# Kernel tuning notes

Measured on AMD Instinct MI355X. Metric: run time of the kernel, lower is better.

The kernel has to match this reference:

```python
import jax, jax.numpy as jnp
import numpy as np

KS = 3
N = KS ** 3  # 27 kernel taps
EPS = 1e-5

def conv3d(x, w, stride=1, padding=0):
    return jax.lax.conv_general_dilated(
        x, w, (stride,) * 3, [(padding, padding)] * 3,
        dimension_numbers=('NCDHW', 'OIDHW', 'NCDHW'))

def batchnorm(x, gamma, beta):
    mu = jnp.mean(x, axis=(0, 2, 3, 4), keepdims=True)
    var = jnp.var(x, axis=(0, 2, 3, 4), keepdims=True)
    return (x - mu) * jax.lax.rsqrt(var + EPS) * gamma[None, :, None, None, None] + beta[None, :, None, None, None]

def deform_conv3d(x, w_p, b_p, w_m, b_m, w_dc):
    b, c, D, H, W = x.shape
    offset = conv3d(x, w_p, padding=1) + b_p[None, :, None, None, None]      # (b,3N,D,H,W)
    m = jax.nn.sigmoid(conv3d(x, w_m, padding=1) + b_m[None, :, None, None, None])  # (b,N,D,H,W)
    x_pad = jnp.pad(x, ((0, 0), (0, 0), (1, 1), (1, 1), (1, 1)))
    Dp, Hp, Wp = D + 2, H + 2, W + 2
    r = jnp.arange(-(KS - 1) // 2, KS // 2 + 1, dtype=x.dtype)
    pn_d, pn_h, pn_w = [a.reshape(-1) for a in jnp.meshgrid(r, r, r, indexing='ij')]
    off = offset.transpose(0, 2, 3, 4, 1)                                    # (b,D,H,W,3N)
    p0_d = jnp.arange(1, D + 1, dtype=x.dtype)[:, None, None, None]
    p0_h = jnp.arange(1, H + 1, dtype=x.dtype)[None, :, None, None]
    p0_w = jnp.arange(1, W + 1, dtype=x.dtype)[None, None, :, None]
    pd = p0_d + pn_d + off[..., :N]
    ph = p0_h + pn_h + off[..., N:2 * N]
    pw = p0_w + pn_w + off[..., 2 * N:]
    d0 = jnp.clip(jnp.floor(pd), 0.0, Dp - 1.0); d1 = jnp.clip(d0 + 1.0, 0.0, Dp - 1.0)
    h0 = jnp.clip(jnp.floor(ph), 0.0, Hp - 1.0); h1 = jnp.clip(h0 + 1.0, 0.0, Hp - 1.0)
    w0 = jnp.clip(jnp.floor(pw), 0.0, Wp - 1.0); w1 = jnp.clip(w0 + 1.0, 0.0, Wp - 1.0)
    pd = jnp.clip(pd, 0.0, Dp - 1.0); ph = jnp.clip(ph, 0.0, Hp - 1.0); pw = jnp.clip(pw, 0.0, Wp - 1.0)
    xf = x_pad.reshape(b, c, -1)
    def gather(qd, qh, qw):
        idx = (qd * (Hp * Wp) + qh * Wp + qw).astype(jnp.int32).reshape(b, 1, -1)
        v = jnp.take_along_axis(xf, jnp.broadcast_to(idx, (b, c, idx.shape[-1])), axis=2)
        return v.reshape(b, c, D, H, W, N)
    x_off = jnp.zeros((b, c, D, H, W, N), x.dtype)
    for qd, wd in ((d0, 1.0 + d0 - pd), (d1, 1.0 - d1 + pd)):
        for qh, wh in ((h0, 1.0 + h0 - ph), (h1, 1.0 - h1 + ph)):
            for qw, ww in ((w0, 1.0 + w0 - pw), (w1, 1.0 - w1 + pw)):
                x_off = x_off + (wd * wh * ww)[:, None] * gather(qd, qh, qw)
    x_off = x_off * m.transpose(0, 2, 3, 4, 1)[:, None]                      # modulation
    # interleave kernel taps: (b,c,D,kd,H,kh,W,kw) -> (b,c,D*KS,H*KS,W*KS)
    x_off = x_off.reshape(b, c, D, H, W, KS, KS, KS)
    x_off = x_off.transpose(0, 1, 2, 5, 3, 6, 4, 7).reshape(b, c, D * KS, H * KS, W * KS)
    out = conv3d(x_off, w_dc, stride=KS)
    p = jnp.concatenate([pd, ph, pw], axis=-1)                               # (b,D,H,W,3N)
    return out, p

def setup_inputs() -> dict:
    key = jax.random.key(0)
    ks = jax.random.split(key, 10)
    B, D = 4, 48
    return {
        'x': jax.random.normal(ks[0], (B, 1, D, D, D), jnp.float32),
        'w_p': jax.random.normal(ks[1], (3 * N, 1, KS, KS, KS), jnp.float32) * 0.05,
        'b_p': jnp.zeros((3 * N,), jnp.float32),
        'w_m': jax.random.normal(ks[2], (N, 1, KS, KS, KS), jnp.float32) * 0.1,
        'b_m': jnp.zeros((N,), jnp.float32),
        'w_dc': jax.random.normal(ks[3], (1, 1, KS, KS, KS), jnp.float32) * 0.2,
        'g_d': jnp.ones((1,), jnp.float32), 'be_d': jnp.zeros((1,), jnp.float32),
        'w_c1': jax.random.normal(ks[4], (32, 1, KS, KS, KS), jnp.float32) * 0.3,
        'g1': jnp.ones((32,), jnp.float32), 'be1': jnp.zeros((32,), jnp.float32),
        'w_c2': jax.random.normal(ks[5], (64, 32, KS, KS, KS), jnp.float32) * 0.06,
        'g2': jnp.ones((64,), jnp.float32), 'be2': jnp.zeros((64,), jnp.float32),
        'w_fc': jax.random.normal(ks[6], (10, 64), jnp.float32) * 0.1,
        'b_fc': jnp.zeros((10,), jnp.float32),
    }

def reference(x, w_p, b_p, w_m, b_m, w_dc, g_d, be_d, w_c1, g1, be1, w_c2, g2, be2, w_fc, b_fc):
    inp = x
    for _ in range(2):
        y, p = deform_conv3d(inp, w_p, b_p, w_m, b_m, w_dc)
        xxx = y
        inp = jax.nn.relu(batchnorm(y, g_d, be_d))
    h = jax.nn.relu(batchnorm(conv3d(inp, w_c1, padding=1), g1, be1))
    h = jax.nn.relu(batchnorm(conv3d(h, w_c2, padding=1), g2, be2))
    h = jax.lax.reduce_window(h, -jnp.inf, jax.lax.max, (1, 1, 3, 3, 3), (1, 1, 3, 3, 3), 'VALID')
    h = h.mean(axis=(2, 3, 4))                       # adaptive avg pool to 1
    logits = h @ w_fc.T + b_fc
    return logits, xxx, p
```

## Files before the change

kernel.cpp:

```cpp
#include <hip/hip_runtime.h>
#include <math.h>

#define BSZ 4
#define DD 48
#define SS (48*48*48)
#define NV (BSZ*SS)
#define PS 125000
#define EPSBN 1e-5f

typedef __attribute__((ext_vector_type(8))) short bf16x8;
typedef __attribute__((ext_vector_type(4))) short s16x4;
typedef __attribute__((ext_vector_type(4))) float f32x4;

__device__ __forceinline__ short f2b(float f){
  unsigned u = __float_as_uint(f);
  u = (u + 0x7FFFu + ((u>>16)&1u)) >> 16;
  return (short)u;
}
__device__ __forceinline__ float b2f(short s){
  return __uint_as_float(((unsigned)(unsigned short)s)<<16);
}

__global__ __launch_bounds__(256) void pad_kernel(
    const float* __restrict__ src, float* __restrict__ dst)
{
  int idx = blockIdx.x*256 + threadIdx.x;
  if (idx >= BSZ*PS) return;
  int b = idx / PS; int r = idx - b*PS;
  int z = r/2500; int r2 = r - z*2500; int yy = r2/50; int xx = r2 - yy*50;
  float v = 0.f;
  if (z>=1 && z<=48 && yy>=1 && yy<=48 && xx>=1 && xx<=48)
    v = src[(size_t)b*SS + (size_t)((z-1)*48 + (yy-1))*48 + (xx-1)];
  dst[idx] = v;
}

__global__ void woff2_kernel(const float* __restrict__ w_p, const float* __restrict__ b_p,
                             const float* __restrict__ w_m, const float* __restrict__ b_m,
                             short* __restrict__ wo2)
{
  int o = blockIdx.x*256 + threadIdx.x;
  if (o >= 112*32) return;
  int k = o & 31; int c = o >> 5;
  int f = c >> 4, qq = (c >> 2) & 3, r = c & 3;
  int n = 4*f + qq;
  float v = 0.f;
  if (n < 27){
    if (k < 27)       v = (r < 3) ? w_p[(r*27+n)*27 + k] : w_m[n*27 + k];
    else if (k == 27) v = (r < 3) ? b_p[r*27+n]          : b_m[n];
  }
  wo2[o] = f2b(v);
}

template<bool WRITE_P>
__global__ __launch_bounds__(256) void deform3_kernel(
    const float* __restrict__ xpad,
    const short* __restrict__ wo2,
    const float* __restrict__ w_dc,
    float* __restrict__ y, float* __restrict__ p_out)
{
  __shared__ short xt[6*6*18];
  __shared__ __align__(16) float pbuf[WRITE_P ? 64*81 : 4];

  int bid = blockIdx.x;
  int bw = bid % 3; int bh = (bid/3)%12; int bd = (bid/36)%12; int b = bid/432;
  int d0 = bd*4, h0 = bh*4, w0 = bw*16;
  int tid = threadIdx.x;
  const float* xp = xpad + (size_t)b*PS;

  for (int e = tid; e < 648; e += 256){
    int z = e/108; int rem = e - z*108; int yy = rem/18; int xx = rem - yy*18;
    xt[e] = f2b(xp[(d0+z)*2500 + (h0+yy)*50 + (w0+xx)]);
  }
  __syncthreads();

  int lane = tid & 63, wid = tid >> 6;
  int q = lane >> 4, n16 = lane & 15;

  bf16x8 aF[7];
  #pragma unroll
  for (int f=0; f<7; ++f)
    aF[f] = *(const bf16x8*)(wo2 + (f*16 + n16)*32 + q*8);

  int toffs[8];
  #pragma unroll
  for (int j=0;j<8;++j){
    int t = q*8 + j; int tc = t > 26 ? 0 : t;
    int kd = tc/9, rr = tc - kd*9, kh = rr/3, kw = rr - kh*3;
    toffs[j] = kd*108 + kh*18 + kw;
  }

  float wdcv[7], fkd[7], fkh[7], fkw[7];
  #pragma unroll
  for (int f=0; f<7; ++f){
    int n = 4*f + q;
    if (n < 27){
      int kd = n/9, rr = n - kd*9, kh = rr/3, kw = rr - kh*3;
      wdcv[f] = w_dc[n];
      fkd[f] = (float)kd; fkh[f] = (float)kh; fkw[f] = (float)kw;
    } else { wdcv[f]=0.f; fkd[f]=0.f; fkh[f]=0.f; fkw[f]=0.f; }
  }

  const short one_bf = (short)0x3F80;
  const f32x4 zero4 = {0.f,0.f,0.f,0.f};
  float based = (float)(d0 + wid);
  float basew = (float)(w0 + n16);

  #pragma unroll 1
  for (int dy=0; dy<4; ++dy){
    int vbase = wid*108 + dy*18 + n16;
    bf16x8 bF;
    #pragma unroll
    for (int j=0;j<8;++j){
      short xv = xt[vbase + toffs[j]];
      bF[j] = (j<3 || q<3) ? xv : one_bf;
    }
    f32x4 acc[7];
    #pragma unroll
    for (int f=0; f<7; ++f)
      acc[f] = __builtin_amdgcn_mfma_f32_16x16x32_bf16(aF[f], bF, zero4, 0,0,0);

    float baseh = (float)(h0 + dy);
    float accv = 0.f;
    #pragma unroll
    for (int f=0; f<7; ++f){
      int n = 4*f + q;
      if (n < 27){
        float od = acc[f][0], oh = acc[f][1], ow = acc[f][2], mr = acc[f][3];
        float mm = __builtin_amdgcn_rcpf(1.f + __expf(-mr));
        float pdv = based + fkd[f] + od;
        float phv = baseh + fkh[f] + oh;
        float pwv = basew + fkw[f] + ow;
        float fd0 = fminf(fmaxf(floorf(pdv),0.f),49.f), fd1 = fminf(fd0+1.f,49.f);
        float pdc = fminf(fmaxf(pdv,0.f),49.f);
        float wd0 = 1.f + fd0 - pdc, wd1 = 1.f - fd1 + pdc;
        float fh0 = fminf(fmaxf(floorf(phv),0.f),49.f), fh1 = fminf(fh0+1.f,49.f);
        float phc = fminf(fmaxf(phv,0.f),49.f);
        float wh0 = 1.f + fh0 - phc, wh1 = 1.f - fh1 + phc;
        float fw0 = fminf(fmaxf(floorf(pwv),0.f),49.f), fw1 = fminf(fw0+1.f,49.f);
        float pwc = fminf(fmaxf(pwv,0.f),49.f);
        float wwa = 1.f + fw0 - pwc, wwb = 1.f - fw1 + pwc;
        int iz0 = (int)fd0*2500, iz1 = (int)fd1*2500;
        int iy0 = (int)fh0*50,   iy1 = (int)fh1*50;
        int ix0 = (int)fw0,      ix1 = (int)fw1;
        float v000=xp[iz0+iy0+ix0], v001=xp[iz0+iy0+ix1];
        float v010=xp[iz0+iy1+ix0], v011=xp[iz0+iy1+ix1];
        float v100=xp[iz1+iy0+ix0], v101=xp[iz1+iy0+ix1];
        float v110=xp[iz1+iy1+ix0], v111=xp[iz1+iy1+ix1];
        float sv = wd0*(wh0*(wwa*v000+wwb*v001)+wh1*(wwa*v010+wwb*v011))
                 + wd1*(wh0*(wwa*v100+wwb*v101)+wh1*(wwa*v110+wwb*v111));
        accv += sv*mm*wdcv[f];
        if constexpr (WRITE_P){
          int vb = (wid*16 + n16)*81;
          pbuf[vb + n]      = pdc;
          pbuf[vb + 27 + n] = phc;
          pbuf[vb + 54 + n] = pwc;
        }
      }
    }
    accv += __shfl_xor(accv, 16);
    accv += __shfl_xor(accv, 32);
    if (q == 0)
      y[(size_t)b*SS + (size_t)((d0+wid)*48 + (h0+dy))*48 + (w0+n16)] = accv;

    if constexpr (WRITE_P){
      __syncthreads();
      size_t rbase = ((((size_t)b*48 + (d0+wid))*48 + (h0+dy))*48 + w0)*81;
      const float* src = pbuf + wid*1296;
      float* dst = p_out + rbase;
      #pragma unroll
      for (int k=0;k<6;++k){
        int i4 = (lane + (k<<6))<<2;
        if (i4 < 1296){
          f32x4 v = *(const f32x4*)(src + i4);
          *(f32x4*)(dst + i4) = v;
        }
      }
      __syncthreads();
    }
  }
}

__global__ __launch_bounds__(256) void bn_stats_kernel(
    const float* __restrict__ x, int nch, float* __restrict__ sums)
{
  int c = blockIdx.y;
  float s1=0.f, s2=0.f;
  for (int i=blockIdx.x*blockDim.x+threadIdx.x; i<NV; i+=gridDim.x*blockDim.x){
    int b=i/SS; int s=i-b*SS;
    float v = x[((size_t)b*nch+c)*SS + s];
    s1+=v; s2+=v*v;
  }
  __shared__ float r1[256], r2[256];
  r1[threadIdx.x]=s1; r2[threadIdx.x]=s2; __syncthreads();
  for (int o=128;o>0;o>>=1){
    if (threadIdx.x<o){ r1[threadIdx.x]+=r1[threadIdx.x+o]; r2[threadIdx.x]+=r2[threadIdx.x+o]; }
    __syncthreads();
  }
  if (threadIdx.x==0){ atomicAdd(&sums[2*c],r1[0]); atomicAdd(&sums[2*c+1],r2[0]); }
}

__global__ __launch_bounds__(256) void bn_relu_kernel(
    const float* __restrict__ x, float* __restrict__ out,
    const float* __restrict__ sums, const float* __restrict__ gamma,
    const float* __restrict__ beta, int nch)
{
  size_t idx = (size_t)blockIdx.x*blockDim.x + threadIdx.x;
  size_t total = (size_t)BSZ*nch*SS;
  if (idx>=total) return;
  int c = (int)((idx/SS)%nch);
  float mu  = sums[2*c]  *(1.f/(float)NV);
  float var = sums[2*c+1]*(1.f/(float)NV) - mu*mu;
  float v = (x[idx]-mu)*rsqrtf(var+EPSBN)*gamma[c]+beta[c];
  out[idx] = fmaxf(v,0.f);
}

__global__ __launch_bounds__(256) void conv1c_kernel(
    const float* __restrict__ x, const float* __restrict__ wt, short* __restrict__ out)
{
  __shared__ float sw[32*27];
  for (int i=threadIdx.x;i<32*27;i+=blockDim.x) sw[i]=wt[i];
  __syncthreads();
  int idx = blockIdx.x*blockDim.x + threadIdx.x;
  if (idx >= NV) return;
  int b = idx / SS; int s = idx - b*SS;
  int d = s / (DD*DD); int r2 = s - d*DD*DD; int h = r2/DD; int w = r2 - h*DD;
  const float* xb = x + (size_t)b*SS;
  float nb[27];
  #pragma unroll
  for (int kd=0;kd<3;++kd)
  #pragma unroll
  for (int kh=0;kh<3;++kh)
  #pragma unroll
  for (int kw=0;kw<3;++kw){
    int zz=d+kd-1, yy=h+kh-1, xx=w+kw-1;
    bool ok = ((unsigned)zz<48u)&&((unsigned)yy<48u)&&((unsigned)xx<48u);
    nb[kd*9+kh*3+kw] = ok ? xb[(zz*48+yy)*48+xx] : 0.f;
  }
  #pragma unroll 1
  for (int g8=0; g8<4; ++g8){
    bf16x8 vv;
    #pragma unroll
    for (int cc=0; cc<8; ++cc){
      int c = g8*8 + cc;
      float a=0.f;
      #pragma unroll
      for (int t=0;t<27;++t) a = fmaf(sw[c*27+t], nb[t], a);
      vv[cc] = f2b(a);
    }
    *(bf16x8*)(out + (size_t)idx*32 + g8*8) = vv;
  }
}

template<int NCH>
__global__ __launch_bounds__(256) void bn_stats_cl(
    const short* __restrict__ x, float* __restrict__ sums)
{
  constexpr int GPB = NCH/8;
  const long NG = (long)NV*GPB;
  int tid = threadIdx.x;
  f32x4 sa = {0.f,0.f,0.f,0.f}, sb = sa, qa = sa, qb = sa;
  for (long g = (long)blockIdx.x*256+tid; g < NG; g += (long)gridDim.x*256){
    bf16x8 v8 = *(const bf16x8*)(x + g*8);
    float v;
    v=b2f(v8[0]); sa[0]+=v; qa[0]+=v*v;
    v=b2f(v8[1]); sa[1]+=v; qa[1]+=v*v;
    v=b2f(v8[2]); sa[2]+=v; qa[2]+=v*v;
    v=b2f(v8[3]); sa[3]+=v; qa[3]+=v*v;
    v=b2f(v8[4]); sb[0]+=v; qb[0]+=v*v;
    v=b2f(v8[5]); sb[1]+=v; qb[1]+=v*v;
    v=b2f(v8[6]); sb[2]+=v; qb[2]+=v*v;
    v=b2f(v8[7]); sb[3]+=v; qb[3]+=v*v;
  }
  #pragma unroll
  for (int m = GPB; m < 64; m <<= 1){
    sa[0]+=__shfl_xor(sa[0],m); sa[1]+=__shfl_xor(sa[1],m);
    sa[2]+=__shfl_xor(sa[2],m); sa[3]+=__shfl_xor(sa[3],m);
    sb[0]+=__shfl_xor(sb[0],m); sb[1]+=__shfl_xor(sb[1],m);
    sb[2]+=__shfl_xor(sb[2],m); sb[3]+=__shfl_xor(sb[3],m);
    qa[0]+=__shfl_xor(qa[0],m); qa[1]+=__shfl_xor(qa[1],m);
    qa[2]+=__shfl_xor(qa[2],m); qa[3]+=__shfl_xor(qa[3],m);
    qb[0]+=__shfl_xor(qb[0],m); qb[1]+=__shfl_xor(qb[1],m);
    qb[2]+=__shfl_xor(qb[2],m); qb[3]+=__shfl_xor(qb[3],m);
  }
  int lane = tid & 63, wid = tid >> 6;
  __shared__ float red[4][GPB][16];
  if (lane < GPB){
    red[wid][lane][0]=sa[0];  red[wid][lane][1]=sa[1];
    red[wid][lane][2]=sa[2];  red[wid][lane][3]=sa[3];
    red[wid][lane][4]=sb[0];  red[wid][lane][5]=sb[1];
    red[wid][lane][6]=sb[2];  red[wid][lane][7]=sb[3];
    red[wid][lane][8]=qa[0];  red[wid][lane][9]=qa[1];
    red[wid][lane][10]=qa[2]; red[wid][lane][11]=qa[3];
    red[wid][lane][12]=qb[0]; red[wid][lane][13]=qb[1];
    red[wid][lane][14]=qb[2]; red[wid][lane][15]=qb[3];
  }
  __syncthreads();
  if (tid < GPB*16){
    int gi = tid >> 4, v = tid & 15;
    float t = red[0][gi][v] + red[1][gi][v] + red[2][gi][v] + red[3][gi][v];
    int ch = gi*8 + (v & 7);
    atomicAdd(&sums[2*ch + (v>>3)], t);
  }
}

__global__ __launch_bounds__(256) void bn_relu_cl32(
    short* __restrict__ x, const float* __restrict__ sums,
    const float* __restrict__ gamma, const float* __restrict__ beta)
{
  __shared__ float ssc[32], ssh[32];
  int tid = threadIdx.x;
  if (tid < 32){
    float mu  = sums[2*tid]  *(1.f/(float)NV);
    float var = sums[2*tid+1]*(1.f/(float)NV) - mu*mu;
    float sc = rsqrtf(var+EPSBN)*gamma[tid];
    ssc[tid]=sc; ssh[tid]=beta[tid]-mu*sc;
  }
  __syncthreads();
  long g = (long)blockIdx.x*256 + tid;
  int cb = ((int)(g&3))*8;
  bf16x8 v8 = *(bf16x8*)(x + g*8);
  #pragma unroll
  for (int j=0;j<8;++j){
    float v = fmaxf(fmaf(b2f(v8[j]), ssc[cb+j], ssh[cb+j]), 0.f);
    v8[j] = f2b(v);
  }
  *(bf16x8*)(x + g*8) = v8;
}

__global__ __launch_bounds__(256) void conv2_mfma2(
    const short* __restrict__ h1c, const short* __restrict__ wbf,
    short* __restrict__ t2c)
{
  __shared__ __align__(16) short slab[4*648*8];
  int bid0 = blockIdx.x;
  int bid = (bid0 & 7)*216 + (bid0 >> 3);
  int bw = bid % 3; int bh = (bid/3)%12; int bd = (bid/36)%12; int b = bid/432;
  int d0 = bd*4, h0 = bh*4, w0 = bw*16;
  int tid = threadIdx.x;
  const short* hb = h1c + (size_t)b*SS*32;

  for (int e = tid; e < 648; e += 256){
    int z = e/108; int rem = e - z*108; int y = rem/18; int x = rem - y*18;
    int gd = d0-1+z, gh = h0-1+y, gw = w0-1+x;
    bool ok = ((unsigned)gd<48u)&&((unsigned)gh<48u)&&((unsigned)gw<48u);
    bf16x8 v0 = {0,0,0,0,0,0,0,0}, v1=v0, v2=v0, v3=v0;
    if (ok){
      const bf16x8* src = (const bf16x8*)(hb + (size_t)((gd*48+gh)*48+gw)*32);
      v0=src[0]; v1=src[1]; v2=src[2]; v3=src[3];
    }
    *(bf16x8*)&slab[(0*648+e)*8] = v0;
    *(bf16x8*)&slab[(1*648+e)*8] = v1;
    *(bf16x8*)&slab[(2*648+e)*8] = v2;
    *(bf16x8*)&slab[(3*648+e)*8] = v3;
  }
  __syncthreads();

  int lane = tid & 63, wid = tid >> 6;
  int q = lane >> 4, n16 = lane & 15;
  f32x4 zero4 = {0.f,0.f,0.f,0.f};
  f32x4 acc[4][4];
  #pragma unroll
  for (int i=0;i<4;++i)
  #pragma unroll
  for (int j=0;j<4;++j) acc[i][j] = zero4;

  #pragma unroll 1
  for (int tap=0; tap<27; ++tap){
    int kd = tap/9; int kh = (tap/3)%3; int kw = tap%3;
    const short* wp = wbf + (size_t)tap*64*32 + n16*32 + q*8;
    bf16x8 aF[4];
    #pragma unroll
    for (int mb=0; mb<4; ++mb)
      aF[mb] = *(const bf16x8*)(wp + mb*16*32);

    int zz = wid + kd;
    #pragma unroll
    for (int dy=0; dy<4; ++dy){
      int e = (zz*6 + (dy+kh))*18 + (n16+kw);
      bf16x8 bF = *(const bf16x8*)&slab[(q*648 + e)*8];
      #pragma unroll
      for (int mb=0; mb<4; ++mb)
        acc[mb][dy] = __builtin_amdgcn_mfma_f32_16x16x32_bf16(aF[mb], bF, acc[mb][dy], 0,0,0);
    }
  }

  short* tb = t2c + (size_t)b*SS*64;
  #pragma unroll
  for (int dy=0; dy<4; ++dy){
    int svox = ((d0+wid)*48 + (h0+dy))*48 + (w0+n16);
    #pragma unroll
    for (int mb=0; mb<4; ++mb){
      s16x4 o4;
      #pragma unroll
      for (int r=0;r<4;++r) o4[r] = f2b(acc[mb][dy][r]);
      *(s16x4*)(tb + (size_t)svox*64 + mb*16 + q*4) = o4;
    }
  }
}

__global__ void wconv_kernel(const float* __restrict__ w, short* __restrict__ wbf)
{
  int o = blockIdx.x*blockDim.x + threadIdx.x;
  if (o >= 27*64*32) return;
  int ci = o & 31; int co = (o>>5) & 63; int tap = o >> 11;
  wbf[o] = f2b(w[(co*32+ci)*27 + tap]);
}

__global__ __launch_bounds__(128) void pool64c_kernel(
    const short* __restrict__ t2c, const float* __restrict__ sums,
    const float* __restrict__ gamma, const float* __restrict__ beta,
    float* __restrict__ pooled)
{
  __shared__ float ssc[64], ssh[64];
  int tid = threadIdx.x;
  if (tid < 64){
    float mu  = sums[2*tid]  *(1.f/(float)NV);
    float var = sums[2*tid+1]*(1.f/(float)NV) - mu*mu;
    float sc = rsqrtf(var+EPSBN)*gamma[tid];
    ssc[tid]=sc; ssh[tid]=beta[tid]-mu*sc;
  }
  __syncthreads();
  int b = blockIdx.z, pd = blockIdx.y, ph = blockIdx.x;
  int c8 = tid & 7, pw = tid >> 3;
  const short* tb = t2c + (size_t)b*SS*64;
  f32x4 mxa = {-1e30f,-1e30f,-1e30f,-1e30f}, mxb = mxa;
  float sc0=ssc[c8*8+0], sc1=ssc[c8*8+1], sc2=ssc[c8*8+2], sc3=ssc[c8*8+3];
  float sc4=ssc[c8*8+4], sc5=ssc[c8*8+5], sc6=ssc[c8*8+6], sc7=ssc[c8*8+7];
  float sh0=ssh[c8*8+0], sh1=ssh[c8*8+1], sh2=ssh[c8*8+2], sh3=ssh[c8*8+3];
  float sh4=ssh[c8*8+4], sh5=ssh[c8*8+5], sh6=ssh[c8*8+6], sh7=ssh[c8*8+7];
  #pragma unroll
  for (int kd=0;kd<3;++kd)
  #pragma unroll 1
  for (int kh=0;kh<3;++kh)
  #pragma unroll
  for (int kw=0;kw<3;++kw){
    int vox = ((pd*3+kd)*48 + (ph*3+kh))*48 + (pw*3+kw);
    bf16x8 v8 = *(const bf16x8*)(tb + (size_t)vox*64 + c8*8);
    float v;
    v = fmaxf(fmaf(b2f(v8[0]), sc0, sh0), 0.f); mxa[0] = fmaxf(mxa[0], v);
    v = fmaxf(fmaf(b2f(v8[1]), sc1, sh1), 0.f); mxa[1] = fmaxf(mxa[1], v);
    v = fmaxf(fmaf(b2f(v8[2]), sc2, sh2), 0.f); mxa[2] = fmaxf(mxa[2], v);
    v = fmaxf(fmaf(b2f(v8[3]), sc3, sh3), 0.f); mxa[3] = fmaxf(mxa[3], v);
    v = fmaxf(fmaf(b2f(v8[4]), sc4, sh4), 0.f); mxb[0] = fmaxf(mxb[0], v);
    v = fmaxf(fmaf(b2f(v8[5]), sc5, sh5), 0.f); mxb[1] = fmaxf(mxb[1], v);
    v = fmaxf(fmaf(b2f(v8[6]), sc6, sh6), 0.f); mxb[2] = fmaxf(mxb[2], v);
    v = fmaxf(fmaf(b2f(v8[7]), sc7, sh7), 0.f); mxb[3] = fmaxf(mxb[3], v);
  }
  __shared__ float r[128][8];
  r[tid][0]=mxa[0]; r[tid][1]=mxa[1]; r[tid][2]=mxa[2]; r[tid][3]=mxa[3];
  r[tid][4]=mxb[0]; r[tid][5]=mxb[1]; r[tid][6]=mxb[2]; r[tid][7]=mxb[3];
  __syncthreads();
  for (int o=64;o>=8;o>>=1){
    if (tid<o){
      #pragma unroll
      for (int j=0;j<8;++j) r[tid][j]+=r[tid+o][j];
    }
    __syncthreads();
  }
  if (tid<8){
    #pragma unroll
    for (int j=0;j<8;++j) atomicAdd(&pooled[b*64 + tid*8 + j], r[tid][j]);
  }
}

__global__ void fc_kernel(const float* __restrict__ pooled,
                          const float* __restrict__ w_fc, const float* __restrict__ b_fc,
                          float* __restrict__ logits)
{
  int t = threadIdx.x;
  if (t < 40){
    int b = t/10, k = t - 10*(t/10);
    float a = b_fc[k];
    #pragma unroll 1
    for (int c=0;c<64;++c) a = fmaf(pooled[b*64+c]*(1.f/4096.f), w_fc[k*64+c], a);
    logits[b*10+k] = a;
  }
}

extern "C" void kernel_launch(void* const* d_in, const int* in_sizes, int n_in,
                              void* d_out, int out_size, void* d_ws, size_t ws_size,
                              hipStream_t stream)
{
  const float* x    = (const float*)d_in[0];
  const float* w_p  = (const float*)d_in[1];
  const float* b_p  = (const float*)d_in[2];
  const float* w_m  = (const float*)d_in[3];
  const float* b_m  = (const float*)d_in[4];
  const float* w_dc = (const float*)d_in[5];
  const float* g_d  = (const float*)d_in[6];
  const float* be_d = (const float*)d_in[7];
  const float* w_c1 = (const float*)d_in[8];
  const float* g1   = (const float*)d_in[9];
  const float* be1  = (const float*)d_in[10];
  const float* w_c2 = (const float*)d_in[11];
  const float* g2   = (const float*)d_in[12];
  const float* be2  = (const float*)d_in[13];
  const float* w_fc = (const float*)d_in[14];
  const float* b_fc = (const float*)d_in[15];

  float* out    = (float*)d_out;
  float* logits = out;
  float* xxx    = out + 40;
  float* p_out  = out + 40 + NV;

  float* ws     = (float*)d_ws;
  float* inp    = ws;
  float* stats  = inp + NV;
  float* pooled = stats + 128;
  short* wbf    = (short*)(pooled + 256);
  short* wo2    = wbf + 27*64*32;
  float* xpad   = (float*)(wo2 + 112*32);
  short* h1c    = (short*)(xpad + (size_t)BSZ*PS);
  short* t2c    = h1c + (size_t)NV*32;
  float* y1     = (float*)t2c;

  const int nblk = (NV + 255)/256;
  const int pblk = (BSZ*PS + 255)/256;

  wconv_kernel<<<(27*64*32+255)/256,256,0,stream>>>(w_c2, wbf);
  woff2_kernel<<<(112*32+255)/256,256,0,stream>>>(w_p, b_p, w_m, b_m, wo2);

  pad_kernel<<<pblk,256,0,stream>>>(x, xpad);
  deform3_kernel<false><<<1728,256,0,stream>>>(xpad, wo2, w_dc, y1, nullptr);
  hipMemsetAsync(stats, 0, 2*sizeof(float), stream);
  bn_stats_kernel<<<dim3(64,1),256,0,stream>>>(y1, 1, stats);
  bn_relu_kernel<<<nblk,256,0,stream>>>(y1, inp, stats, g_d, be_d, 1);

  pad_kernel<<<pblk,256,0,stream>>>(inp, xpad);
  deform3_kernel<true><<<1728,256,0,stream>>>(xpad, wo2, w_dc, xxx, p_out);
  hipMemsetAsync(stats, 0, 2*sizeof(float), stream);
  bn_stats_kernel<<<dim3(64,1),256,0,stream>>>(xxx, 1, stats);
  bn_relu_kernel<<<nblk,256,0,stream>>>(xxx, inp, stats, g_d, be_d, 1);

  conv1c_kernel<<<nblk,256,0,stream>>>(inp, w_c1, h1c);
  hipMemsetAsync(stats, 0, 64*sizeof(float), stream);
  bn_stats_cl<32><<<256,256,0,stream>>>(h1c, stats);
  bn_relu_cl32<<<NV*4/256,256,0,stream>>>(h1c, stats, g1, be1);

  conv2_mfma2<<<1728,256,0,stream>>>(h1c, wbf, t2c);
  hipMemsetAsync(stats, 0, 128*sizeof(float), stream);
  bn_stats_cl<64><<<512,256,0,stream>>>(t2c, stats);
  hipMemsetAsync(pooled, 0, 256*sizeof(float), stream);
  pool64c_kernel<<<dim3(16,16,BSZ),128,0,stream>>>(t2c, stats, g2, be2, pooled);

  fc_kernel<<<1,64,0,stream>>>(pooled, w_fc, b_fc, logits);
}
```

Before: 406.3 us.

## Fuse BN stats into deform conv, BN+pad, MFMA conv1, BN into conv2 load

Deform conv kernels now accumulate BN sum and sum-of-squares through wave shuffles and per-block atomics, so the separate stats passes go away. BN+ReLU is fused with the padding kernel, and conv1 is rewritten as a bf16 MFMA kernel reading the padded tile. The layer-1 BN+ReLU pass over h1c is folded into conv2's shared-memory slab load. These changes remove several full-tensor read/write passes and launches, at the cost of bf16 rounding of conv1 inputs and more atomics.

```diff
diff --git a/kernel.cpp b/kernel.cpp
--- a/kernel.cpp
+++ b/kernel.cpp
@@ -32,6 +32,27 @@
   if (z>=1 && z<=48 && yy>=1 && yy<=48 && xx>=1 && xx<=48)
     v = src[(size_t)b*SS + (size_t)((z-1)*48 + (yy-1))*48 + (xx-1)];
   dst[idx] = v;
+}
+
+__global__ __launch_bounds__(256) void bnpad_kernel(
+    const float* __restrict__ y, const float* __restrict__ st,
+    const float* __restrict__ gamma, const float* __restrict__ beta,
+    float* __restrict__ xpad)
+{
+  int idx = blockIdx.x*256 + threadIdx.x;
+  if (idx >= BSZ*PS) return;
+  float mu  = st[0]*(1.f/(float)NV);
+  float var = st[1]*(1.f/(float)NV) - mu*mu;
+  float sc  = rsqrtf(var+EPSBN)*gamma[0];
+  float sh  = beta[0] - mu*sc;
+  int b = idx / PS; int r = idx - b*PS;
+  int z = r/2500; int r2 = r - z*2500; int yy = r2/50; int xx = r2 - yy*50;
+  float v = 0.f;
+  if (z>=1 && z<=48 && yy>=1 && yy<=48 && xx>=1 && xx<=48){
+    float t = y[(size_t)b*SS + (size_t)((z-1)*48 + (yy-1))*48 + (xx-1)];
+    v = fmaxf(fmaf(t, sc, sh), 0.f);
+  }
+  xpad[idx] = v;
 }
 
 __global__ void woff2_kernel(const float* __restrict__ w_p, const float* __restrict__ b_p,
@@ -51,15 +72,25 @@
   wo2[o] = f2b(v);
 }
 
+__global__ void wconv1_kernel(const float* __restrict__ w, short* __restrict__ wb)
+{
+  int o = blockIdx.x*256 + threadIdx.x;
+  if (o >= 32*32) return;
+  int k = o & 31; int c = o >> 5;
+  wb[o] = f2b(k < 27 ? w[c*27 + k] : 0.f);
+}
+
 template<bool WRITE_P>
 __global__ __launch_bounds__(256) void deform3_kernel(
     const float* __restrict__ xpad,
     const short* __restrict__ wo2,
     const float* __restrict__ w_dc,
-    float* __restrict__ y, float* __restrict__ p_out)
+    float* __restrict__ y, float* __restrict__ p_out,
+    float* __restrict__ st)
 {
   __shared__ short xt[6*6*18];
   __shared__ __align__(16) float pbuf[WRITE_P ? 64*81 : 4];
+  __shared__ float yred[8];
 
   int bid = blockIdx.x;
   int bw = bid % 3; int bh = (bid/3)%12; int bd = (bid/36)%12; int b = bid/432;
@@ -104,6 +135,7 @@
   const f32x4 zero4 = {0.f,0.f,0.f,0.f};
   float based = (float)(d0 + wid);
   float basew = (float)(w0 + n16);
+  float ys = 0.f, yq = 0.f;
 
   #pragma unroll 1
   for (int dy=0; dy<4; ++dy){
@@ -159,8 +191,10 @@
     }
     accv += __shfl_xor(accv, 16);
     accv += __shfl_xor(accv, 32);
-    if (q == 0)
+    if (q == 0){
       y[(size_t)b*SS + (size_t)((d0+wid)*48 + (h0+dy))*48 + (w0+n16)] = accv;
+      ys += accv; yq += accv*accv;
+    }
 
     if constexpr (WRITE_P){
       __syncthreads();
@@ -178,76 +212,63 @@
       __syncthreads();
     }
   }
-}
-
-__global__ __launch_bounds__(256) void bn_stats_kernel(
-    const float* __restrict__ x, int nch, float* __restrict__ sums)
-{
-  int c = blockIdx.y;
-  float s1=0.f, s2=0.f;
-  for (int i=blockIdx.x*blockDim.x+threadIdx.x; i<NV; i+=gridDim.x*blockDim.x){
-    int b=i/SS; int s=i-b*SS;
-    float v = x[((size_t)b*nch+c)*SS + s];
-    s1+=v; s2+=v*v;
-  }
-  __shared__ float r1[256], r2[256];
-  r1[threadIdx.x]=s1; r2[threadIdx.x]=s2; __syncthreads();
-  for (int o=128;o>0;o>>=1){
-    if (threadIdx.x<o){ r1[threadIdx.x]+=r1[threadIdx.x+o]; r2[threadIdx.x]+=r2[threadIdx.x+o]; }
-    __syncthreads();
-  }
-  if (threadIdx.x==0){ atomicAdd(&sums[2*c],r1[0]); atomicAdd(&sums[2*c+1],r2[0]); }
-}
-
-__global__ __launch_bounds__(256) void bn_relu_kernel(
-    const float* __restrict__ x, float* __restrict__ out,
-    const float* __restrict__ sums, const float* __restrict__ gamma,
-    const float* __restrict__ beta, int nch)
-{
-  size_t idx = (size_t)blockIdx.x*blockDim.x + threadIdx.x;
-  size_t total = (size_t)BSZ*nch*SS;
-  if (idx>=total) return;
-  int c = (int)((idx/SS)%nch);
-  float mu  = sums[2*c]  *(1.f/(float)NV);
-  float var = sums[2*c+1]*(1.f/(float)NV) - mu*mu;
-  float v = (x[idx]-mu)*rsqrtf(var+EPSBN)*gamma[c]+beta[c];
-  out[idx] = fmaxf(v,0.f);
-}
-
-__global__ __launch_bounds__(256) void conv1c_kernel(
-    const float* __restrict__ x, const float* __restrict__ wt, short* __restrict__ out)
-{
-  __shared__ float sw[32*27];
-  for (int i=threadIdx.x;i<32*27;i+=blockDim.x) sw[i]=wt[i];
-  __syncthreads();
-  int idx = blockIdx.x*blockDim.x + threadIdx.x;
-  if (idx >= NV) return;
-  int b = idx / SS; int s = idx - b*SS;
-  int d = s / (DD*DD); int r2 = s - d*DD*DD; int h = r2/DD; int w = r2 - h*DD;
-  const float* xb = x + (size_t)b*SS;
-  float nb[27];
-  #pragma unroll
-  for (int kd=0;kd<3;++kd)
-  #pragma unroll
-  for (int kh=0;kh<3;++kh)
-  #pragma unroll
-  for (int kw=0;kw<3;++kw){
-    int zz=d+kd-1, yy=h+kh-1, xx=w+kw-1;
-    bool ok = ((unsigned)zz<48u)&&((unsigned)yy<48u)&&((unsigned)xx<48u);
-    nb[kd*9+kh*3+kw] = ok ? xb[(zz*48+yy)*48+xx] : 0.f;
-  }
-  #pragma unroll 1
-  for (int g8=0; g8<4; ++g8){
-    bf16x8 vv;
-    #pragma unroll
-    for (int cc=0; cc<8; ++cc){
-      int c = g8*8 + cc;
-      float a=0.f;
-      #pragma unroll
-      for (int t=0;t<27;++t) a = fmaf(sw[c*27+t], nb[t], a);
-      vv[cc] = f2b(a);
-    }
-    *(bf16x8*)(out + (size_t)idx*32 + g8*8) = vv;
+
+  ys += __shfl_xor(ys, 1); ys += __shfl_xor(ys, 2);
+  ys += __shfl_xor(ys, 4); ys += __shfl_xor(ys, 8);
+  yq += __shfl_xor(yq, 1); yq += __shfl_xor(yq, 2);
+  yq += __shfl_xor(yq, 4); yq += __shfl_xor(yq, 8);
+  if (lane == 0){ yred[wid] = ys; yred[4+wid] = yq; }
+  __syncthreads();
+  if (tid == 0) atomicAdd(&st[0], yred[0]+yred[1]+yred[2]+yred[3]);
+  if (tid == 1) atomicAdd(&st[1], yred[4]+yred[5]+yred[6]+yred[7]);
+}
+
+__global__ __launch_bounds__(256) void conv1m_kernel(
+    const float* __restrict__ xpad, const short* __restrict__ wc1b,
+    short* __restrict__ h1c)
+{
+  __shared__ short xt[6*6*18];
+  int bid = blockIdx.x;
+  int bw = bid % 3; int bh = (bid/3)%12; int bd = (bid/36)%12; int b = bid/432;
+  int d0 = bd*4, h0 = bh*4, w0 = bw*16;
+  int tid = threadIdx.x;
+  const float* xp = xpad + (size_t)b*PS;
+
+  for (int e = tid; e < 648; e += 256){
+    int z = e/108; int rem = e - z*108; int yy = rem/18; int xx = rem - yy*18;
+    xt[e] = f2b(xp[(d0+z)*2500 + (h0+yy)*50 + (w0+xx)]);
+  }
+  __syncthreads();
+
+  int lane = tid & 63, wid = tid >> 6;
+  int q = lane >> 4, n16 = lane & 15;
+
+  bf16x8 aF0 = *(const bf16x8*)(wc1b + n16*32 + q*8);
+  bf16x8 aF1 = *(const bf16x8*)(wc1b + (16+n16)*32 + q*8);
+
+  int toffs[8];
+  #pragma unroll
+  for (int j=0;j<8;++j){
+    int t = q*8 + j; int tc = t > 26 ? 0 : t;
+    int kd = tc/9, rr = tc - kd*9, kh = rr/3, kw = rr - kh*3;
+    toffs[j] = kd*108 + kh*18 + kw;
+  }
+
+  const f32x4 zero4 = {0.f,0.f,0.f,0.f};
+  #pragma unroll
+  for (int dy=0; dy<4; ++dy){
+    int vbase = wid*108 + dy*18 + n16;
+    bf16x8 bF;
+    #pragma unroll
+    for (int j=0;j<8;++j) bF[j] = xt[vbase + toffs[j]];
+    f32x4 a0 = __builtin_amdgcn_mfma_f32_16x16x32_bf16(aF0, bF, zero4, 0,0,0);
+    f32x4 a1 = __builtin_amdgcn_mfma_f32_16x16x32_bf16(aF1, bF, zero4, 0,0,0);
+    size_t idx = (size_t)b*SS + (size_t)((d0+wid)*48 + (h0+dy))*48 + (w0+n16);
+    s16x4 o0, o1;
+    #pragma unroll
+    for (int r=0;r<4;++r){ o0[r]=f2b(a0[r]); o1[r]=f2b(a1[r]); }
+    *(s16x4*)(h1c + idx*32 + q*4)      = o0;
+    *(s16x4*)(h1c + idx*32 + 16 + q*4) = o1;
   }
 }
 
@@ -303,55 +324,50 @@
   }
 }
 
-__global__ __launch_bounds__(256) void bn_relu_cl32(
-    short* __restrict__ x, const float* __restrict__ sums,
-    const float* __restrict__ gamma, const float* __restrict__ beta)
-{
+__global__ __launch_bounds__(256) void conv2_mfma2(
+    const short* __restrict__ h1c, const short* __restrict__ wbf,
+    const float* __restrict__ st1, const float* __restrict__ g1,
+    const float* __restrict__ be1, short* __restrict__ t2c)
+{
+  __shared__ __align__(16) short slab[4*648*8];
   __shared__ float ssc[32], ssh[32];
   int tid = threadIdx.x;
   if (tid < 32){
-    float mu  = sums[2*tid]  *(1.f/(float)NV);
-    float var = sums[2*tid+1]*(1.f/(float)NV) - mu*mu;
-    float sc = rsqrtf(var+EPSBN)*gamma[tid];
-    ssc[tid]=sc; ssh[tid]=beta[tid]-mu*sc;
-  }
-  __syncthreads();
-  long g = (long)blockIdx.x*256 + tid;
-  int cb = ((int)(g&3))*8;
-  bf16x8 v8 = *(bf16x8*)(x + g*8);
-  #pragma unroll
-  for (int j=0;j<8;++j){
-    float v = fmaxf(fmaf(b2f(v8[j]), ssc[cb+j], ssh[cb+j]), 0.f);
-    v8[j] = f2b(v);
-  }
-  *(bf16x8*)(x + g*8) = v8;
-}
-
-__global__ __launch_bounds__(256) void conv2_mfma2(
-    const short* __restrict__ h1c, const short* __restrict__ wbf,
-    short* __restrict__ t2c)
-{
-  __shared__ __align__(16) short slab[4*648*8];
+    float mu  = st1[2*tid]  *(1.f/(float)NV);
+    float var = st1[2*tid+1]*(1.f/(float)NV) - mu*mu;
+    float sc = rsqrtf(var+EPSBN)*g1[tid];
+    ssc[tid]=sc; ssh[tid]=be1[tid]-mu*sc;
+  }
+  __syncthreads();
+
   int bid0 = blockIdx.x;
   int bid = (bid0 & 7)*216 + (bid0 >> 3);
   int bw = bid % 3; int bh = (bid/3)%12; int bd = (bid/36)%12; int b = bid/432;
   int d0 = bd*4, h0 = bh*4, w0 = bw*16;
-  int tid = threadIdx.x;
   const short* hb = h1c + (size_t)b*SS*32;
 
   for (int e = tid; e < 648; e += 256){
     int z = e/108; int rem = e - z*108; int y = rem/18; int x = rem - y*18;
     int gd = d0-1+z, gh = h0-1+y, gw = w0-1+x;
     bool ok = ((unsigned)gd<48u)&&((unsigned)gh<48u)&&((unsigned)gw<48u);
-    bf16x8 v0 = {0,0,0,0,0,0,0,0}, v1=v0, v2=v0, v3=v0;
     if (ok){
       const bf16x8* src = (const bf16x8*)(hb + (size_t)((gd*48+gh)*48+gw)*32);
-      v0=src[0]; v1=src[1]; v2=src[2]; v3=src[3];
-    }
-    *(bf16x8*)&slab[(0*648+e)*8] = v0;
-    *(bf16x8*)&slab[(1*648+e)*8] = v1;
-    *(bf16x8*)&slab[(2*648+e)*8] = v2;
-    *(bf16x8*)&slab[(3*648+e)*8] = v3;
+      #pragma unroll
+      for (int g8=0; g8<4; ++g8){
+        bf16x8 raw = src[g8];
+        bf16x8 outv;
+        #pragma unroll
+        for (int j=0;j<8;++j){
+          float v = fmaxf(fmaf(b2f(raw[j]), ssc[g8*8+j], ssh[g8*8+j]), 0.f);
+          outv[j] = f2b(v);
+        }
+        *(bf16x8*)&slab[(g8*648+e)*8] = outv;
+      }
+    } else {
+      bf16x8 zz = {0,0,0,0,0,0,0,0};
+      #pragma unroll
+      for (int g8=0; g8<4; ++g8) *(bf16x8*)&slab[(g8*648+e)*8] = zz;
+    }
   }
   __syncthreads();
 
@@ -504,44 +520,42 @@
   float* p_out  = out + 40 + NV;
 
   float* ws     = (float*)d_ws;
-  float* inp    = ws;
-  float* stats  = inp + NV;
-  float* pooled = stats + 128;
+  float* stats  = ws;
+  float* pooled = stats + 512;
   short* wbf    = (short*)(pooled + 256);
   short* wo2    = wbf + 27*64*32;
-  float* xpad   = (float*)(wo2 + 112*32);
-  short* h1c    = (short*)(xpad + (size_t)BSZ*PS);
+  short* wc1b   = wo2 + 112*32;
+  float* xpad   = (float*)(wc1b + 32*32);
+  float* y1     = xpad + (size_t)BSZ*PS;
+  short* h1c    = (short*)(y1 + NV);
   short* t2c    = h1c + (size_t)NV*32;
-  float* y1     = (float*)t2c;
-
-  const int nblk = (NV + 255)/256;
+
+  float* st_y1 = stats + 0;
+  float* st_y2 = stats + 2;
+  float* st_h1 = stats + 4;
+  float* st_t2 = stats + 68;
+
   const int pblk = (BSZ*PS + 255)/256;
+
+  hipMemsetAsync(stats, 0, (512+256)*sizeof(float), stream);
 
   wconv_kernel<<<(27*64*32+255)/256,256,0,stream>>>(w_c2, wbf);
   woff2_kernel<<<(112*32+255)/256,256,0,stream>>>(w_p, b_p, w_m, b_m, wo2);
+  wconv1_kernel<<<(32*32+255)/256,256,0,stream>>>(w_c1, wc1b);
 
   pad_kernel<<<pblk,256,0,stream>>>(x, xpad);
-  deform3_kernel<false><<<1728,256,0,stream>>>(xpad, wo2, w_dc, y1, nullptr);
-  hipMemsetAsync(stats, 0, 2*sizeof(float), stream);
-  bn_stats_kernel<<<dim3(64,1),256,0,stream>>>(y1, 1, stats);
-  bn_relu_kernel<<<nblk,256,0,stream>>>(y1, inp, stats, g_d, be_d, 1);
-
-  pad_kernel<<<pblk,256,0,stream>>>(inp, xpad);
-  deform3_kernel<true><<<1728,256,0,stream>>>(xpad, wo2, w_dc, xxx, p_out);
-  hipMemsetAsync(stats, 0, 2*sizeof(float), stream);
-  bn_stats_kernel<<<dim3(64,1),256,0,stream>>>(xxx, 1, stats);
-  bn_relu_kernel<<<nblk,256,0,stream>>>(xxx, inp, stats, g_d, be_d, 1);
-
-  conv1c_kernel<<<nblk,256,0,stream>>>(inp, w_c1, h1c);
-  hipMemsetAsync(stats, 0, 64*sizeof(float), stream);
-  bn_stats_cl<32><<<256,256,0,stream>>>(h1c, stats);
-  bn_relu_cl32<<<NV*4/256,256,0,stream>>>(h1c, stats, g1, be1);
-
-  conv2_mfma2<<<1728,256,0,stream>>>(h1c, wbf, t2c);
-  hipMemsetAsync(stats, 0, 128*sizeof(float), stream);
-  bn_stats_cl<64><<<512,256,0,stream>>>(t2c, stats);
-  hipMemsetAsync(pooled, 0, 256*sizeof(float), stream);
-  pool64c_kernel<<<dim3(16,16,BSZ),128,0,stream>>>(t2c, stats, g2, be2, pooled);
+  deform3_kernel<false><<<1728,256,0,stream>>>(xpad, wo2, w_dc, y1, nullptr, st_y1);
+  bnpad_kernel<<<pblk,256,0,stream>>>(y1, st_y1, g_d, be_d, xpad);
+
+  deform3_kernel<true><<<1728,256,0,stream>>>(xpad, wo2, w_dc, xxx, p_out, st_y2);
+  bnpad_kernel<<<pblk,256,0,stream>>>(xxx, st_y2, g_d, be_d, xpad);
+
+  conv1m_kernel<<<1728,256,0,stream>>>(xpad, wc1b, h1c);
+  bn_stats_cl<32><<<256,256,0,stream>>>(h1c, st_h1);
+
+  conv2_mfma2<<<1728,256,0,stream>>>(h1c, wbf, st_h1, g1, be1, t2c);
+  bn_stats_cl<64><<<512,256,0,stream>>>(t2c, st_t2);
+  pool64c_kernel<<<dim3(16,16,BSZ),128,0,stream>>>(t2c, st_t2, g2, be2, pooled);
 
   fc_kernel<<<1,64,0,stream>>>(pooled, w_fc, b_fc, logits);
 }
```

New measurement: 374.6 us. 7.8% less time.
